# Performance work log

Measured on AMD Instinct MI355X. Metric: run time of the kernel, lower is better.

The kernel has to match this reference:

```python
import jax, jax.numpy as jnp
import numpy as np

EPS = 1e-8

def setup_inputs() -> dict:
    key = jax.random.key(0)
    k1, k2, k3, k4 = jax.random.split(key, 4)
    B, S, D = 64, 512, 512
    emb1 = jax.random.normal(k1, (B, S, D), dtype=jnp.float32)
    emb2 = jax.random.normal(k2, (B, S, D), dtype=jnp.float32)
    # contiguous prefix attention masks (first n tokens valid), as assumed by the original
    len1 = jax.random.randint(k3, (B,), S // 4, S + 1)
    len2 = jax.random.randint(k4, (B,), S // 4, S + 1)
    pos = jnp.arange(S)
    mask1 = (pos[None, :] < len1[:, None]).astype(jnp.int32)
    mask2 = (pos[None, :] < len2[:, None]).astype(jnp.int32)
    return {"article_1_emb": emb1, "article_2_emb": emb2,
            "article_1_att_mask": mask1, "article_2_att_mask": mask2}


def reference(article_1_emb, article_2_emb, article_1_att_mask, article_2_att_mask):
    # L2-normalize token embeddings (cosine similarity = dot of normalized vectors)
    def l2n(x):
        n = jnp.sqrt(jnp.sum(x * x, axis=-1, keepdims=True))
        return x / jnp.maximum(n, EPS)

    e1 = l2n(article_1_emb)   # [B, S1, D]
    e2 = l2n(article_2_emb)   # [B, S2, D]
    sim = jnp.einsum('bid,bjd->bij', e1, e2)  # [B, S1, S2] pairwise cosine sims

    m1 = article_1_att_mask.astype(jnp.bool_)  # [B, S1]
    m2 = article_2_att_mask.astype(jnp.bool_)  # [B, S2]
    NEG = jnp.float32(-1e9)

    # max over valid j for each valid i, and max over valid i for each valid j
    row_max = jnp.max(jnp.where(m2[:, None, :], sim, NEG), axis=2)  # [B, S1]
    col_max = jnp.max(jnp.where(m1[:, :, None], sim, NEG), axis=1)  # [B, S2]
    row_sum = jnp.sum(jnp.where(m1, row_max, 0.0), axis=1)          # [B]
    col_sum = jnp.sum(jnp.where(m2, col_max, 0.0), axis=1)          # [B]

    n1 = jnp.sum(article_1_att_mask, axis=1).astype(jnp.float32)
    n2 = jnp.sum(article_2_att_mask, axis=1).astype(jnp.float32)
    return (row_sum + col_sum) / (n1 + n2)
```

## Files before the change

kernel.cpp:

```cpp
#include <hip/hip_runtime.h>
#include <hip/hip_bf16.h>


typedef __attribute__((ext_vector_type(8))) short bf16x8;
typedef __attribute__((ext_vector_type(4))) float f32x4;

#define NEGBIG (-1e9f)

__device__ __forceinline__ unsigned packbf2_hw(float lo, float hi) {
    __hip_bfloat162 h = __float22bfloat162_rn(float2{lo, hi});
    union { __hip_bfloat162 h; unsigned u; } c; c.h = h;
    return c.u;
}

__global__ __launch_bounds__(256)
void sim_fused(const float* __restrict__ e1, const float* __restrict__ e2,
               const int* __restrict__ m1g, const int* __restrict__ m2g,
               float* __restrict__ rowmax_p,
               float* __restrict__ colmax_p)
{
    const int rt  = blockIdx.x;
    const int ct  = blockIdx.y;
    const int b   = blockIdx.z;
    const int tid = threadIdx.x;
    const int lane = tid & 63;
    const int w    = tid >> 6;
    const int wm   = w >> 1;
    const int wn   = w & 1;
    const int q    = lane >> 4;
    const int ln   = lane & 15;
    const int nb   = ct * 128;

    __shared__ __align__(16) ushort sA[2][128 * 32];
    __shared__ __align__(16) ushort sB[2][128 * 32];
    __shared__ float spr[2][128];
    __shared__ float spc[2][128];
    __shared__ int   sm1[128], sm2[128];
    __shared__ float sinv1[128], sinv2[128];

    if (tid < 128) sm1[tid] = m1g[b * 512 + rt * 128 + tid];
    else           sm2[tid - 128] = m2g[b * 512 + nb + (tid - 128)];

    const int r = tid >> 1;
    const int h = tid & 1;
    const int s = (r ^ (r >> 2)) & 3;
    const float* gA = e1 + ((size_t)(b * 512 + rt * 128 + r)) * 512 + h * 16;
    const float* gB = e2 + ((size_t)(b * 512 + nb + r)) * 512 + h * 16;
    const int wo0 = r * 32 + (((2 * h)     ^ s) << 3);
    const int wo1 = r * 32 + (((2 * h + 1) ^ s) << 3);

    const int sln = (ln & 3) ^ ((ln >> 2) & 3);
    int aoff[4], boff[4];
    #pragma unroll
    for (int mt = 0; mt < 4; ++mt)
        aoff[mt] = (wm * 64 + mt * 16 + ln) * 32 + ((q ^ sln) << 3);
    #pragma unroll
    for (int nt = 0; nt < 4; ++nt)
        boff[nt] = (wn * 64 + nt * 16 + ln) * 32 + ((q ^ sln) << 3);

    float ssA = 0.f, ssB = 0.f;
    float4 ra[4], rb[4];

    auto LOADK = [&](int kf) {
        const float4* pa = reinterpret_cast<const float4*>(gA + kf);
        const float4* pb = reinterpret_cast<const float4*>(gB + kf);
        ra[0] = pa[0]; ra[1] = pa[1]; ra[2] = pa[2]; ra[3] = pa[3];
        rb[0] = pb[0]; rb[1] = pb[1]; rb[2] = pb[2]; rb[3] = pb[3];
    };
    auto CVTWRITE = [&](int p) {
        #pragma unroll
        for (int i = 0; i < 4; ++i) {
            ssA += ra[i].x * ra[i].x + ra[i].y * ra[i].y
                 + ra[i].z * ra[i].z + ra[i].w * ra[i].w;
            ssB += rb[i].x * rb[i].x + rb[i].y * rb[i].y
                 + rb[i].z * rb[i].z + rb[i].w * rb[i].w;
        }
        uint4 u;
        u.x = packbf2_hw(ra[0].x, ra[0].y); u.y = packbf2_hw(ra[0].z, ra[0].w);
        u.z = packbf2_hw(ra[1].x, ra[1].y); u.w = packbf2_hw(ra[1].z, ra[1].w);
        *reinterpret_cast<uint4*>(&sA[p][wo0]) = u;
        u.x = packbf2_hw(ra[2].x, ra[2].y); u.y = packbf2_hw(ra[2].z, ra[2].w);
        u.z = packbf2_hw(ra[3].x, ra[3].y); u.w = packbf2_hw(ra[3].z, ra[3].w);
        *reinterpret_cast<uint4*>(&sA[p][wo1]) = u;
        u.x = packbf2_hw(rb[0].x, rb[0].y); u.y = packbf2_hw(rb[0].z, rb[0].w);
        u.z = packbf2_hw(rb[1].x, rb[1].y); u.w = packbf2_hw(rb[1].z, rb[1].w);
        *reinterpret_cast<uint4*>(&sB[p][wo0]) = u;
        u.x = packbf2_hw(rb[2].x, rb[2].y); u.y = packbf2_hw(rb[2].z, rb[2].w);
        u.z = packbf2_hw(rb[3].x, rb[3].y); u.w = packbf2_hw(rb[3].z, rb[3].w);
        *reinterpret_cast<uint4*>(&sB[p][wo1]) = u;
    };

    f32x4 acc[4][4];
    #pragma unroll
    for (int i = 0; i < 4; ++i)
        #pragma unroll
        for (int j = 0; j < 4; ++j)
            acc[i][j] = (f32x4){0.f, 0.f, 0.f, 0.f};

    LOADK(0);
    CVTWRITE(0);
    LOADK(32);
    __syncthreads();

    #pragma unroll 2
    for (int k = 0; k < 16; ++k) {
        const int p = k & 1;
        bf16x8 af[4], bfr[4];
        #pragma unroll
        for (int mt = 0; mt < 4; ++mt)
            af[mt] = *reinterpret_cast<const bf16x8*>(&sA[p][aoff[mt]]);
        #pragma unroll
        for (int nt = 0; nt < 4; ++nt)
            bfr[nt] = *reinterpret_cast<const bf16x8*>(&sB[p][boff[nt]]);
        if (k < 15) CVTWRITE(p ^ 1);
        if (k < 14) LOADK((k + 2) * 32);
        #pragma unroll
        for (int mt = 0; mt < 4; ++mt)
            #pragma unroll
            for (int nt = 0; nt < 4; ++nt)
                acc[mt][nt] = __builtin_amdgcn_mfma_f32_16x16x32_bf16(
                    af[mt], bfr[nt], acc[mt][nt], 0, 0, 0);
        __syncthreads();
    }

    ssA += __shfl_xor(ssA, 1);
    ssB += __shfl_xor(ssB, 1);
    if (h == 0) {
        sinv1[r] = 1.0f / fmaxf(sqrtf(ssA), 1e-8f);
        sinv2[r] = 1.0f / fmaxf(sqrtf(ssB), 1e-8f);
    }
    __syncthreads();

    float invj[4];
    f32x4 invi[4];
    #pragma unroll
    for (int nt = 0; nt < 4; ++nt)
        invj[nt] = sinv2[wn * 64 + nt * 16 + ln];
    #pragma unroll
    for (int mt = 0; mt < 4; ++mt)
        #pragma unroll
        for (int rg = 0; rg < 4; ++rg)
            invi[mt][rg] = sinv1[wm * 64 + mt * 16 + q * 4 + rg];
    #pragma unroll
    for (int mt = 0; mt < 4; ++mt)
        #pragma unroll
        for (int nt = 0; nt < 4; ++nt)
            acc[mt][nt] = acc[mt][nt] * (invi[mt] * invj[nt]);

    #pragma unroll
    for (int mt = 0; mt < 4; ++mt) {
        #pragma unroll
        for (int rg = 0; rg < 4; ++rg) {
            float rm = NEGBIG;
            #pragma unroll
            for (int nt = 0; nt < 4; ++nt) {
                float v = sm2[wn * 64 + nt * 16 + ln] ? acc[mt][nt][rg] : NEGBIG;
                rm = fmaxf(rm, v);
            }
            rm = fmaxf(rm, __shfl_xor(rm, 1));
            rm = fmaxf(rm, __shfl_xor(rm, 2));
            rm = fmaxf(rm, __shfl_xor(rm, 4));
            rm = fmaxf(rm, __shfl_xor(rm, 8));
            if (ln == 0) spr[wn][wm * 64 + mt * 16 + q * 4 + rg] = rm;
        }
    }
    #pragma unroll
    for (int nt = 0; nt < 4; ++nt) {
        float cm = NEGBIG;
        #pragma unroll
        for (int mt = 0; mt < 4; ++mt)
            #pragma unroll
            for (int rg = 0; rg < 4; ++rg) {
                float v = sm1[wm * 64 + mt * 16 + q * 4 + rg] ? acc[mt][nt][rg] : NEGBIG;
                cm = fmaxf(cm, v);
            }
        cm = fmaxf(cm, __shfl_xor(cm, 16));
        cm = fmaxf(cm, __shfl_xor(cm, 32));
        if (lane < 16) spc[wm][wn * 64 + nt * 16 + ln] = cm;
    }
    __syncthreads();
    if (tid < 128) {
        rowmax_p[((size_t)b * 4 + ct) * 512 + rt * 128 + tid] =
            fmaxf(spr[0][tid], spr[1][tid]);
        colmax_p[((size_t)b * 4 + rt) * 512 + nb + tid] =
            fmaxf(spc[0][tid], spc[1][tid]);
    }
}

__global__ __launch_bounds__(256)
void final_kernel(const int* __restrict__ m1g, const int* __restrict__ m2g,
                  const float* __restrict__ rowmax_p, const float* __restrict__ colmax_p,
                  float* __restrict__ out)
{
    const int b = blockIdx.x;
    const int tid = threadIdx.x;
    const int lane = tid & 63;
    const int w = tid >> 6;

    float sum = 0.f;
    float nn  = 0.f;
    for (int j = tid; j < 512; j += 256) {
        int mm1 = m1g[b * 512 + j];
        int mm2 = m2g[b * 512 + j];
        nn += (float)(mm1 + mm2);
        const float* rp = rowmax_p + (size_t)b * 2048 + j;
        float rm = fmaxf(fmaxf(rp[0], rp[512]), fmaxf(rp[1024], rp[1536]));
        if (mm1) sum += rm;
        const float* cp = colmax_p + (size_t)b * 2048 + j;
        float cm = fmaxf(fmaxf(cp[0], cp[512]), fmaxf(cp[1024], cp[1536]));
        if (mm2) sum += cm;
    }
    #pragma unroll
    for (int m = 32; m; m >>= 1) {
        sum += __shfl_xor(sum, m);
        nn  += __shfl_xor(nn, m);
    }
    __shared__ float ssum[4], snn[4];
    if (lane == 0) { ssum[w] = sum; snn[w] = nn; }
    __syncthreads();
    if (tid == 0) {
        float S = ssum[0] + ssum[1] + ssum[2] + ssum[3];
        float N = snn[0] + snn[1] + snn[2] + snn[3];
        out[b] = S / N;
    }
}

extern "C" void kernel_launch(void* const* d_in, const int* in_sizes, int n_in,
                              void* d_out, int out_size, void* d_ws, size_t ws_size,
                              hipStream_t stream) {
    const float* e1 = (const float*)d_in[0];
    const float* e2 = (const float*)d_in[1];
    const int*   m1 = (const int*)d_in[2];
    const int*   m2 = (const int*)d_in[3];
    float* out = (float*)d_out;

    float* ws = (float*)d_ws;
    float* rowmax_p = ws;
    float* colmax_p = ws + 131072;

    sim_fused<<<dim3(4, 4, 64), 256, 0, stream>>>(e1, e2, m1, m2,
                                                  rowmax_p, colmax_p);
    final_kernel<<<64, 256, 0, stream>>>(m1, m2, rowmax_p, colmax_p, out);
}
```

Before: 187.6 us.

## Double-buffer global prefetch registers and use a custom LDS-only barrier

```diff
diff --git a/kernel.cpp b/kernel.cpp
--- a/kernel.cpp
+++ b/kernel.cpp
@@ -12,6 +12,12 @@
     union { __hip_bfloat162 h; unsigned u; } c; c.h = h;
     return c.u;
 }
+
+#define BAR() do {                                            \
+        asm volatile("s_waitcnt lgkmcnt(0)" ::: "memory");    \
+        __builtin_amdgcn_s_barrier();                         \
+        asm volatile("" ::: "memory");                        \
+    } while (0)
 
 __global__ __launch_bounds__(256)
 void sim_fused(const float* __restrict__ e1, const float* __restrict__ e2,
@@ -33,13 +39,12 @@
 
     __shared__ __align__(16) ushort sA[2][128 * 32];
     __shared__ __align__(16) ushort sB[2][128 * 32];
-    __shared__ float spr[2][128];
-    __shared__ float spc[2][128];
-    __shared__ int   sm1[128], sm2[128];
-    __shared__ float sinv1[128], sinv2[128];
-
-    if (tid < 128) sm1[tid] = m1g[b * 512 + rt * 128 + tid];
-    else           sm2[tid - 128] = m2g[b * 512 + nb + (tid - 128)];
+    float* spr   = reinterpret_cast<float*>(&sA[0][0]);
+    float* spc   = reinterpret_cast<float*>(&sA[0][512]);
+    int*   sm1   = reinterpret_cast<int*>(&sA[0][1024]);
+    int*   sm2   = reinterpret_cast<int*>(&sA[0][1280]);
+    float* sinv1 = reinterpret_cast<float*>(&sB[0][0]);
+    float* sinv2 = reinterpret_cast<float*>(&sB[0][256]);
 
     const int r = tid >> 1;
     const int h = tid & 1;
@@ -59,35 +64,35 @@
         boff[nt] = (wn * 64 + nt * 16 + ln) * 32 + ((q ^ sln) << 3);
 
     float ssA = 0.f, ssB = 0.f;
-    float4 ra[4], rb[4];
-
-    auto LOADK = [&](int kf) {
+    float4 ra[2][4], rb[2][4];
+
+    auto LOADK = [&](int u, int kf) {
         const float4* pa = reinterpret_cast<const float4*>(gA + kf);
         const float4* pb = reinterpret_cast<const float4*>(gB + kf);
-        ra[0] = pa[0]; ra[1] = pa[1]; ra[2] = pa[2]; ra[3] = pa[3];
-        rb[0] = pb[0]; rb[1] = pb[1]; rb[2] = pb[2]; rb[3] = pb[3];
+        ra[u][0] = pa[0]; ra[u][1] = pa[1]; ra[u][2] = pa[2]; ra[u][3] = pa[3];
+        rb[u][0] = pb[0]; rb[u][1] = pb[1]; rb[u][2] = pb[2]; rb[u][3] = pb[3];
     };
-    auto CVTWRITE = [&](int p) {
+    auto CVTWRITE = [&](int u, int pd) {
         #pragma unroll
         for (int i = 0; i < 4; ++i) {
-            ssA += ra[i].x * ra[i].x + ra[i].y * ra[i].y
-                 + ra[i].z * ra[i].z + ra[i].w * ra[i].w;
-            ssB += rb[i].x * rb[i].x + rb[i].y * rb[i].y
-                 + rb[i].z * rb[i].z + rb[i].w * rb[i].w;
+            ssA += ra[u][i].x * ra[u][i].x + ra[u][i].y * ra[u][i].y
+                 + ra[u][i].z * ra[u][i].z + ra[u][i].w * ra[u][i].w;
+            ssB += rb[u][i].x * rb[u][i].x + rb[u][i].y * rb[u][i].y
+                 + rb[u][i].z * rb[u][i].z + rb[u][i].w * rb[u][i].w;
         }
-        uint4 u;
-        u.x = packbf2_hw(ra[0].x, ra[0].y); u.y = packbf2_hw(ra[0].z, ra[0].w);
-        u.z = packbf2_hw(ra[1].x, ra[1].y); u.w = packbf2_hw(ra[1].z, ra[1].w);
-        *reinterpret_cast<uint4*>(&sA[p][wo0]) = u;
-        u.x = packbf2_hw(ra[2].x, ra[2].y); u.y = packbf2_hw(ra[2].z, ra[2].w);
-        u.z = packbf2_hw(ra[3].x, ra[3].y); u.w = packbf2_hw(ra[3].z, ra[3].w);
-        *reinterpret_cast<uint4*>(&sA[p][wo1]) = u;
-        u.x = packbf2_hw(rb[0].x, rb[0].y); u.y = packbf2_hw(rb[0].z, rb[0].w);
-        u.z = packbf2_hw(rb[1].x, rb[1].y); u.w = packbf2_hw(rb[1].z, rb[1].w);
-        *reinterpret_cast<uint4*>(&sB[p][wo0]) = u;
-        u.x = packbf2_hw(rb[2].x, rb[2].y); u.y = packbf2_hw(rb[2].z, rb[2].w);
-        u.z = packbf2_hw(rb[3].x, rb[3].y); u.w = packbf2_hw(rb[3].z, rb[3].w);
-        *reinterpret_cast<uint4*>(&sB[p][wo1]) = u;
+        uint4 v;
+        v.x = packbf2_hw(ra[u][0].x, ra[u][0].y); v.y = packbf2_hw(ra[u][0].z, ra[u][0].w);
+        v.z = packbf2_hw(ra[u][1].x, ra[u][1].y); v.w = packbf2_hw(ra[u][1].z, ra[u][1].w);
+        *reinterpret_cast<uint4*>(&sA[pd][wo0]) = v;
+        v.x = packbf2_hw(ra[u][2].x, ra[u][2].y); v.y = packbf2_hw(ra[u][2].z, ra[u][2].w);
+        v.z = packbf2_hw(ra[u][3].x, ra[u][3].y); v.w = packbf2_hw(ra[u][3].z, ra[u][3].w);
+        *reinterpret_cast<uint4*>(&sA[pd][wo1]) = v;
+        v.x = packbf2_hw(rb[u][0].x, rb[u][0].y); v.y = packbf2_hw(rb[u][0].z, rb[u][0].w);
+        v.z = packbf2_hw(rb[u][1].x, rb[u][1].y); v.w = packbf2_hw(rb[u][1].z, rb[u][1].w);
+        *reinterpret_cast<uint4*>(&sB[pd][wo0]) = v;
+        v.x = packbf2_hw(rb[u][2].x, rb[u][2].y); v.y = packbf2_hw(rb[u][2].z, rb[u][2].w);
+        v.z = packbf2_hw(rb[u][3].x, rb[u][3].y); v.w = packbf2_hw(rb[u][3].z, rb[u][3].w);
+        *reinterpret_cast<uint4*>(&sB[pd][wo1]) = v;
     };
 
     f32x4 acc[4][4];
@@ -97,39 +102,46 @@
         for (int j = 0; j < 4; ++j)
             acc[i][j] = (f32x4){0.f, 0.f, 0.f, 0.f};
 
-    LOADK(0);
-    CVTWRITE(0);
-    LOADK(32);
-    __syncthreads();
-
-    #pragma unroll 2
-    for (int k = 0; k < 16; ++k) {
-        const int p = k & 1;
-        bf16x8 af[4], bfr[4];
-        #pragma unroll
-        for (int mt = 0; mt < 4; ++mt)
-            af[mt] = *reinterpret_cast<const bf16x8*>(&sA[p][aoff[mt]]);
-        #pragma unroll
-        for (int nt = 0; nt < 4; ++nt)
-            bfr[nt] = *reinterpret_cast<const bf16x8*>(&sB[p][boff[nt]]);
-        if (k < 15) CVTWRITE(p ^ 1);
-        if (k < 14) LOADK((k + 2) * 32);
-        #pragma unroll
-        for (int mt = 0; mt < 4; ++mt)
-            #pragma unroll
-            for (int nt = 0; nt < 4; ++nt)
-                acc[mt][nt] = __builtin_amdgcn_mfma_f32_16x16x32_bf16(
-                    af[mt], bfr[nt], acc[mt][nt], 0, 0, 0);
-        __syncthreads();
-    }
-
+    LOADK(0, 0);
+    CVTWRITE(0, 0);
+    LOADK(1, 32);
+    BAR();
+
+#define HALF_ITER(P, K)                                                    \
+    do {                                                                   \
+        if ((K) < 14) LOADK(P, ((K) + 2) * 32);                            \
+        bf16x8 af[4], bfr[4];                                              \
+        _Pragma("unroll")                                                  \
+        for (int mt = 0; mt < 4; ++mt)                                     \
+            af[mt] = *reinterpret_cast<const bf16x8*>(&sA[P][aoff[mt]]);   \
+        _Pragma("unroll")                                                  \
+        for (int nt = 0; nt < 4; ++nt)                                     \
+            bfr[nt] = *reinterpret_cast<const bf16x8*>(&sB[P][boff[nt]]);  \
+        if ((K) < 15) CVTWRITE((P) ^ 1, (P) ^ 1);                          \
+        _Pragma("unroll")                                                  \
+        for (int mt = 0; mt < 4; ++mt)                                     \
+            _Pragma("unroll")                                              \
+            for (int nt = 0; nt < 4; ++nt)                                 \
+                acc[mt][nt] = __builtin_amdgcn_mfma_f32_16x16x32_bf16(     \
+                    af[mt], bfr[nt], acc[mt][nt], 0, 0, 0);                \
+        BAR();                                                             \
+    } while (0)
+
+    for (int kk = 0; kk < 8; ++kk) {
+        HALF_ITER(0, 2 * kk);
+        HALF_ITER(1, 2 * kk + 1);
+    }
+#undef HALF_ITER
+
+    if (tid < 128) sm1[tid] = m1g[b * 512 + rt * 128 + tid];
+    else           sm2[tid - 128] = m2g[b * 512 + nb + (tid - 128)];
     ssA += __shfl_xor(ssA, 1);
     ssB += __shfl_xor(ssB, 1);
     if (h == 0) {
         sinv1[r] = 1.0f / fmaxf(sqrtf(ssA), 1e-8f);
         sinv2[r] = 1.0f / fmaxf(sqrtf(ssB), 1e-8f);
     }
-    __syncthreads();
+    BAR();
 
     float invj[4];
     f32x4 invi[4];
@@ -161,7 +173,7 @@
             rm = fmaxf(rm, __shfl_xor(rm, 2));
             rm = fmaxf(rm, __shfl_xor(rm, 4));
             rm = fmaxf(rm, __shfl_xor(rm, 8));
-            if (ln == 0) spr[wn][wm * 64 + mt * 16 + q * 4 + rg] = rm;
+            if (ln == 0) spr[wn * 128 + wm * 64 + mt * 16 + q * 4 + rg] = rm;
         }
     }
     #pragma unroll
@@ -176,14 +188,14 @@
             }
         cm = fmaxf(cm, __shfl_xor(cm, 16));
         cm = fmaxf(cm, __shfl_xor(cm, 32));
-        if (lane < 16) spc[wm][wn * 64 + nt * 16 + ln] = cm;
-    }
-    __syncthreads();
+        if (lane < 16) spc[wm * 128 + wn * 64 + nt * 16 + ln] = cm;
+    }
+    BAR();
     if (tid < 128) {
         rowmax_p[((size_t)b * 4 + ct) * 512 + rt * 128 + tid] =
-            fmaxf(spr[0][tid], spr[1][tid]);
+            fmaxf(spr[tid], spr[128 + tid]);
         colmax_p[((size_t)b * 4 + rt) * 512 + nb + tid] =
-            fmaxf(spc[0][tid], spc[1][tid]);
+            fmaxf(spc[tid], spc[128 + tid]);
     }
 }
 
```

New measurement: 180.1 us. 1.04x faster.
